# Performance work log

Measured on AMD Instinct MI355X. Metric: run time of the kernel, lower is better.

Reference implementation:

```python
import jax, jax.numpy as jnp
import numpy as np

D_MODEL = 1024
VOCAB = 32000
NUM_HEADS = 3  # MTP steps
NHEAD = 2      # attention heads per encoder layer
D_FF = 2048    # torch TransformerEncoderLayer default dim_feedforward
EPS_RMS = 1e-8
EPS_LN = 1e-5


def rmsnorm(x):
    rms = jnp.sqrt(jnp.mean(x * x, axis=-1, keepdims=True) + EPS_RMS)
    return x / rms


def layernorm(x, g, b):
    m = jnp.mean(x, axis=-1, keepdims=True)
    v = jnp.mean((x - m) ** 2, axis=-1, keepdims=True)
    return (x - m) / jnp.sqrt(v + EPS_LN) * g + b


def encoder_layer_single_token(x, p):
    # x: (..., d). Self-attention over a length-1 sequence: softmax over one key
    # gives attention weight 1, so attn_out = Wo @ (Wv @ x). Post-norm (torch default).
    v = x @ p['Wv'].T + p['bv']
    attn = v @ p['Wo'].T + p['bo']
    x = layernorm(x + attn, p['ln1_g'], p['ln1_b'])
    ff = jax.nn.relu(x @ p['W1'].T + p['b1']) @ p['W2'].T + p['b2']
    x = layernorm(x + ff, p['ln2_g'], p['ln2_b'])
    return x


def setup_inputs() -> dict:
    key = jax.random.key(0)
    ks = jax.random.split(key, 4)
    token_ids = jax.random.randint(ks[0], (4, 512), 0, VOCAB)
    embed = jax.random.normal(ks[1], (VOCAB, D_MODEL), dtype=jnp.float32) * 0.02
    s = 1.0 / np.sqrt(D_MODEL)
    params = []
    kk = ks[2]
    for k in range(NUM_HEADS):
        kk, *sub = jax.random.split(kk, 10)
        p = {
            'Wmerge': jax.random.normal(sub[0], (D_MODEL, 2 * D_MODEL)) * s,
            'bmerge': jnp.zeros((D_MODEL,)),
            'Wv': jax.random.normal(sub[1], (D_MODEL, D_MODEL)) * s,
            'bv': jnp.zeros((D_MODEL,)),
            'Wo': jax.random.normal(sub[2], (D_MODEL, D_MODEL)) * s,
            'bo': jnp.zeros((D_MODEL,)),
            'W1': jax.random.normal(sub[3], (D_FF, D_MODEL)) * s,
            'b1': jnp.zeros((D_FF,)),
            'W2': jax.random.normal(sub[4], (D_MODEL, D_FF)) * (1.0 / np.sqrt(D_FF)),
            'b2': jnp.zeros((D_MODEL,)),
            'ln1_g': jnp.ones((D_MODEL,)), 'ln1_b': jnp.zeros((D_MODEL,)),
            'ln2_g': jnp.ones((D_MODEL,)), 'ln2_b': jnp.zeros((D_MODEL,)),
        }
        params.append(p)
    # flatten params into dict entries layer{k}_{name}
    out = {'token_ids': token_ids, 'embed': embed}
    for k, p in enumerate(params):
        for name, val in p.items():
            out[f'l{k}_{name}'] = val
    return out


def _forward(token_ids, embed, layers):
    B, T = token_ids.shape
    embeds = embed[token_ids]              # (B, T, d)
    n_pos = T - NUM_HEADS                  # positions i = 0 .. T-NUM_HEADS-1
    # vectorize over i: h_prev starts as h0_seq[:, i, :] for all i at once
    idx = jnp.arange(n_pos)
    h_prev = embeds[:, idx, :]             # (B, P, d)
    logits_list = []
    for k in range(NUM_HEADS):
        p = layers[k]
        tok = embeds[:, idx + (k + 1), :]  # (B, P, d) future token embeds
        merged = jnp.concatenate([rmsnorm(h_prev), rmsnorm(tok)], axis=-1)  # (B,P,2d)
        x = merged @ p['Wmerge'].T + p['bmerge']                            # (B,P,d)
        h_curr = encoder_layer_single_token(x, p)
        logits = h_curr @ embed.T          # tied unembed (B,P,V)
        logits_list.append(logits)
        h_prev = h_curr
    # stack -> (B, P, NUM_HEADS, V) matching torch stack(dim=1) per-position then outer list
    return jnp.stack(logits_list, axis=2)


def reference(token_ids, embed,
              l0_Wmerge, l0_bmerge, l0_Wv, l0_bv, l0_Wo, l0_bo, l0_W1, l0_b1, l0_W2, l0_b2, l0_ln1_g, l0_ln1_b, l0_ln2_g, l0_ln2_b,
              l1_Wmerge, l1_bmerge, l1_Wv, l1_bv, l1_Wo, l1_bo, l1_W1, l1_b1, l1_W2, l1_b2, l1_ln1_g, l1_ln1_b, l1_ln2_g, l1_ln2_b,
              l2_Wmerge, l2_bmerge, l2_Wv, l2_bv, l2_Wo, l2_bo, l2_W1, l2_b1, l2_W2, l2_b2, l2_ln1_g, l2_ln1_b, l2_ln2_g, l2_ln2_b):
    names = ['Wmerge', 'bmerge', 'Wv', 'bv', 'Wo', 'bo', 'W1', 'b1', 'W2', 'b2', 'ln1_g', 'ln1_b', 'ln2_g', 'ln2_b']
    vals = [l0_Wmerge, l0_bmerge, l0_Wv, l0_bv, l0_Wo, l0_bo, l0_W1, l0_b1, l0_W2, l0_b2, l0_ln1_g, l0_ln1_b, l0_ln2_g, l0_ln2_b,
            l1_Wmerge, l1_bmerge, l1_Wv, l1_bv, l1_Wo, l1_bo, l1_W1, l1_b1, l1_W2, l1_b2, l1_ln1_g, l1_ln1_b, l1_ln2_g, l1_ln2_b,
            l2_Wmerge, l2_bmerge, l2_Wv, l2_bv, l2_Wo, l2_bo, l2_W1, l2_b1, l2_W2, l2_b2, l2_ln1_g, l2_ln1_b, l2_ln2_g, l2_ln2_b]
    layers = [dict(zip(names, vals[i * 14:(i + 1) * 14])) for i in range(NUM_HEADS)]
    return _forward(token_ids, embed, layers)
```

## Files before the change

### kernel.cpp

```cpp
#include <hip/hip_runtime.h>


#define NPOS   509
#define MROWS  2036
#define MPAD   2048
#define DMODEL 1024

typedef _Float16 f16;
typedef _Float16 f16x8 __attribute__((ext_vector_type(8)));
typedef _Float16 f16x4 __attribute__((ext_vector_type(4)));
typedef float    f32x4 __attribute__((ext_vector_type(4)));

#define MFMA16(a, b, c) __builtin_amdgcn_mfma_f32_16x16x32_f16(a, b, c, 0, 0, 0)
#define VM0   asm volatile("s_waitcnt vmcnt(0)" ::: "memory")
#define VM2   asm volatile("s_waitcnt vmcnt(2)" ::: "memory")
#define VM6   asm volatile("s_waitcnt vmcnt(6)" ::: "memory")
#define LGKM0 asm volatile("s_waitcnt lgkmcnt(0)" ::: "memory")
#define SCHED0 __builtin_amdgcn_sched_barrier(0)
#define BAR   asm volatile("s_barrier" ::: "memory")

__device__ __forceinline__ void gld_lds16(const void* g, void* l) {
  __builtin_amdgcn_global_load_lds(
      (const __attribute__((address_space(1))) void*)g,
      (__attribute__((address_space(3))) void*)l, 16, 0, 0);
}

__global__ __launch_bounds__(256) void conv_f32_f16(const float* __restrict__ src,
                                                    f16* __restrict__ dst, long n) {
  long i = ((long)blockIdx.x * 256 + threadIdx.x) * 8;
  if (i + 8 <= n) {
    float4 a = *(const float4*)(src + i);
    float4 b = *(const float4*)(src + i + 4);
    f16x8 o = {(f16)a.x, (f16)a.y, (f16)a.z, (f16)a.w,
               (f16)b.x, (f16)b.y, (f16)b.z, (f16)b.w};
    *(f16x8*)(dst + i) = o;
  }
}

struct ConvArgs { const float* s[12]; f16* d[12]; long n[12]; };
__global__ __launch_bounds__(256) void conv_many(ConvArgs a) {
  int t = blockIdx.y;
  long i = ((long)blockIdx.x * 256 + threadIdx.x) * 8;
  if (i + 8 <= a.n[t]) {
    const float* src = a.s[t];
    float4 x = *(const float4*)(src + i);
    float4 y = *(const float4*)(src + i + 4);
    f16x8 o = {(f16)x.x, (f16)x.y, (f16)x.z, (f16)x.w,
               (f16)y.x, (f16)y.y, (f16)y.z, (f16)y.w};
    *(f16x8*)(a.d[t] + i) = o;
  }
}

struct TpArgs { const float* s[3]; f16* d[3]; };
__global__ __launch_bounds__(256) void transpose3(TpArgs a) {
  __shared__ float t[32][33];
  int h = blockIdx.z;
  int bx = blockIdx.x * 32, by = blockIdx.y * 32;
  int tx = threadIdx.x & 31, ty = threadIdx.x >> 5;
  const float* src = a.s[h];
  f16* dst = a.d[h];
  #pragma unroll
  for (int r = 0; r < 32; r += 8)
    t[ty + r][tx] = src[(long)(by + ty + r) * 1024 + bx + tx];
  __syncthreads();
  #pragma unroll
  for (int r = 0; r < 32; r += 8)
    dst[(long)(bx + ty + r) * 1024 + by + tx] = (f16)t[tx][ty + r];
}

struct BvoArgs { const float* Wo[3]; const float* bv[3]; const float* bo[3]; float* out[3]; };
__global__ __launch_bounds__(64) void make_bvo3(BvoArgs a) {
  int h = blockIdx.y, r = blockIdx.x, l = threadIdx.x;
  const float* Wo = a.Wo[h];
  const float* bv = a.bv[h];
  float s = 0.0f;
  for (int k = l; k < 1024; k += 64) s += Wo[(long)r * 1024 + k] * bv[k];
  #pragma unroll
  for (int off = 32; off > 0; off >>= 1) s += __shfl_xor(s, off);
  if (l == 0) a.out[h][r] = s + a.bo[h][r];
}

__device__ __forceinline__ float2 block_reduce2(float a, float b) {
  #pragma unroll
  for (int off = 32; off > 0; off >>= 1) {
    a += __shfl_xor(a, off);
    b += __shfl_xor(b, off);
  }
  __shared__ float2 red[4];
  int wv = threadIdx.x >> 6;
  if ((threadIdx.x & 63) == 0) red[wv] = make_float2(a, b);
  __syncthreads();
  float2 r0 = red[0], r1 = red[1], r2 = red[2], r3 = red[3];
  return make_float2(r0.x + r1.x + r2.x + r3.x, r0.y + r1.y + r2.y + r3.y);
}

__global__ __launch_bounds__(256) void merge_rms(const float* __restrict__ hprev,
                                                 const float* __restrict__ embed,
                                                 const int* __restrict__ tok,
                                                 f16* __restrict__ merged, int koff,
                                                 int hsel) {
  int r = blockIdx.x;
  int b = r / NPOS, t = r - b * NPOS;
  int tid = threadIdx.x;
  const float* hrow = (hsel >= 0)
      ? embed + (long)tok[b * 512 + t + hsel] * DMODEL
      : hprev + (long)r * DMODEL;
  float4 hv = ((const float4*)hrow)[tid];
  float4 tv = ((const float4*)(embed + (long)tok[b * 512 + t + koff] * DMODEL))[tid];
  float sh = hv.x * hv.x + hv.y * hv.y + hv.z * hv.z + hv.w * hv.w;
  float st = tv.x * tv.x + tv.y * tv.y + tv.z * tv.z + tv.w * tv.w;
  float2 tot = block_reduce2(sh, st);
  float ih = 1.0f / sqrtf(tot.x * (1.0f / DMODEL) + 1e-8f);
  float it = 1.0f / sqrtf(tot.y * (1.0f / DMODEL) + 1e-8f);
  f16x4 oh = {(f16)(hv.x * ih), (f16)(hv.y * ih), (f16)(hv.z * ih), (f16)(hv.w * ih)};
  f16x4 ot = {(f16)(tv.x * it), (f16)(tv.y * it), (f16)(tv.z * it), (f16)(tv.w * it)};
  *(f16x4*)(merged + (long)r * 2048 + tid * 4) = oh;
  *(f16x4*)(merged + (long)r * 2048 + 1024 + tid * 4) = ot;
}

__global__ __launch_bounds__(256) void add_ln(const float* __restrict__ x,
                                              const float* __restrict__ res,
                                              const float* __restrict__ g,
                                              const float* __restrict__ bb,
                                              float* __restrict__ yf,
                                              f16* __restrict__ yh) {
  int r = blockIdx.x, tid = threadIdx.x;
  float4 a = ((const float4*)(x + (long)r * DMODEL))[tid];
  float4 c = ((const float4*)(res + (long)r * DMODEL))[tid];
  a.x += c.x; a.y += c.y; a.z += c.z; a.w += c.w;
  float s  = a.x + a.y + a.z + a.w;
  float ss = a.x * a.x + a.y * a.y + a.z * a.z + a.w * a.w;
  float2 tot = block_reduce2(s, ss);
  float mean = tot.x * (1.0f / DMODEL);
  float var  = tot.y * (1.0f / DMODEL) - mean * mean;
  float inv  = 1.0f / sqrtf(var + 1e-5f);
  float4 gv = ((const float4*)g)[tid];
  float4 bv = ((const float4*)bb)[tid];
  float y0 = (a.x - mean) * inv * gv.x + bv.x;
  float y1 = (a.y - mean) * inv * gv.y + bv.y;
  float y2 = (a.z - mean) * inv * gv.z + bv.z;
  float y3 = (a.w - mean) * inv * gv.w + bv.w;
  float4 o = {y0, y1, y2, y3};
  ((float4*)(yf + (long)r * DMODEL))[tid] = o;
  f16x4 oh = {(f16)y0, (f16)y1, (f16)y2, (f16)y3};
  *(f16x4*)(yh + (long)r * DMODEL + tid * 4) = oh;
}

template <int HAS_BIAS, int RELU, int WF32, int WF16, int MASK>
__global__ __launch_bounds__(256) void gemm_sm(const f16* __restrict__ A,
                                               const f16* __restrict__ B,
                                               const float* __restrict__ bias,
                                               float* __restrict__ Cf,
                                               f16* __restrict__ Ch,
                                               int K, int N, long ldc, long coff,
                                               int mval, long zsA, long zsB, long zsC) {
  __shared__ __align__(16) f16 sA[3][2048];
  __shared__ __align__(16) f16 sB[3][2048];
  const int tid  = threadIdx.x;
  const int lane = tid & 63, wv = tid >> 6;
  const int wm = wv >> 1, wn = wv & 1;
  const int bm = blockIdx.y, bn = blockIdx.x;
  const int lr = lane & 15, lk = lane >> 4;

  A += (long)blockIdx.z * zsA;
  B += (long)blockIdx.z * zsB;
  Ch += (long)blockIdx.z * zsC;

  const f16* gA = A + ((long)(bm * 64 + (tid >> 2))) * K + (tid & 3) * 8;
  const f16* gB = B + ((long)(bn * 64 + (tid >> 2))) * K + (tid & 3) * 8;

  const int aoff = (wm * 32 + lr) * 32 + lk * 8;
  const int boff = (wn * 32 + lr) * 32 + lk * 8;

  f32x4 acc[2][2] = {};

#define SSTAGE(buf, kt)                                \
  gld_lds16(gA + (long)(kt) * 32, &sA[buf][tid * 8]);  \
  gld_lds16(gB + (long)(kt) * 32, &sB[buf][tid * 8]);

  const int nk = K >> 5;
  SSTAGE(0, 0);
  SSTAGE(1, 1);

  int cur = 0, stg = 2;
  for (int kt = 0; kt < nk; ++kt) {
    if (kt + 1 < nk) { VM2; } else { VM0; }
    BAR;
    if (kt + 2 < nk) { SSTAGE(stg, kt + 2); }
    f16x8 af0 = *(const f16x8*)&sA[cur][aoff];
    f16x8 af1 = *(const f16x8*)&sA[cur][aoff + 512];
    f16x8 bf0 = *(const f16x8*)&sB[cur][boff];
    f16x8 bf1 = *(const f16x8*)&sB[cur][boff + 512];
    acc[0][0] = MFMA16(af0, bf0, acc[0][0]);
    acc[0][1] = MFMA16(af0, bf1, acc[0][1]);
    acc[1][0] = MFMA16(af1, bf0, acc[1][0]);
    acc[1][1] = MFMA16(af1, bf1, acc[1][1]);
    cur = cur == 2 ? 0 : cur + 1;
    stg = stg == 2 ? 0 : stg + 1;
  }
#undef SSTAGE

  const int row0 = bm * 64 + wm * 32 + lk * 4;
  const int col0 = bn * 64 + wn * 32 + lr;
  #pragma unroll
  for (int mi = 0; mi < 2; ++mi) {
    #pragma unroll
    for (int ni = 0; ni < 2; ++ni) {
      int col = col0 + ni * 16;
      float bs = HAS_BIAS ? bias[col] : 0.0f;
      #pragma unroll
      for (int rg = 0; rg < 4; ++rg) {
        int row = row0 + mi * 16 + rg;
        if (!MASK || row < mval) {
          float v = acc[mi][ni][rg] + bs;
          if (RELU) v = v > 0.0f ? v : 0.0f;
          if (WF32) Cf[(long)row * ldc + coff + col] = v;
          if (WF16) Ch[(long)row * N + col] = (f16)v;
        }
      }
    }
  }
}

__global__ __launch_bounds__(256, 2) void gemm256x(const f16* __restrict__ A,
                                                   const f16* __restrict__ B,
                                                   float* __restrict__ C) {
  __shared__ __align__(16) f16 sA[3][8192];
  __shared__ __align__(16) f16 sB[3][4096];
  const int K = 1024;
  const int tid = threadIdx.x;
  const int lane = tid & 63;
  const int wv = tid >> 6;
  const int wm = wv >> 1, wn = wv & 1;
  const int lr = lane & 15, lk = lane >> 4;

  const int flat = blockIdx.y * 250 + blockIdx.x;
  const int xcd = flat & 7, idx = flat >> 3;
  const int bm = xcd * 3 + (idx % 3);
  const int bn = idx / 3;

  const int srow = tid >> 2;
  const int schunk = (tid & 3) ^ ((tid >> 3) & 3);
  const f16* gA = A + (long)(bm * 256 + srow) * K + schunk * 8;
  const f16* gB = B + (long)(bn * 128 + srow) * K + schunk * 8;

  const int swz = ((lr >> 1) & 3) << 3;
  const int aoff = (((wm * 128 + lr) * 32) + lk * 8) ^ swz;
  const int boff = (((wn * 64  + lr) * 32) + lk * 8) ^ swz;

  f32x4 acc[8][4] = {};

#define STG_A(s, kt, i) gld_lds16(gA + (long)(kt) * 32 + (long)(i) * 64 * K, \
                                  &sA[s][(i) * 2048 + tid * 8]);
#define STG_B(s, kt, j) gld_lds16(gB + (long)(kt) * 32 + (long)(j) * 64 * K, \
                                  &sB[s][(j) * 2048 + tid * 8]);
#define STAGE_H1(s, kt) STG_A(s, kt, 0) STG_A(s, kt, 1) STG_B(s, kt, 0)
#define STAGE_H2(s, kt) STG_A(s, kt, 2) STG_A(s, kt, 3) STG_B(s, kt, 1)

  STAGE_H1(0, 0) STAGE_H2(0, 0)
  STAGE_H1(1, 1) STAGE_H2(1, 1)
  VM6; BAR;

  const int nt = 32;
  int slot = 0;
  for (int t = 0; t < nt; ++t) {
    const int s2 = (slot >= 1) ? slot - 1 : slot + 2;
    const int kt2 = (t + 2 < nt) ? (t + 2) : (t + 2 - nt);
    f16x8 alo[4], ahi[4], bf[4];

    STAGE_H1(s2, kt2)
    #pragma unroll
    for (int i = 0; i < 4; ++i) alo[i] = *(const f16x8*)&sA[slot][aoff + i * 512];
    #pragma unroll
    for (int j = 0; j < 4; ++j) bf[j] = *(const f16x8*)&sB[slot][boff + j * 512];
    LGKM0; SCHED0;
    __builtin_amdgcn_s_setprio(1);
    #pragma unroll
    for (int i = 0; i < 4; ++i)
      #pragma unroll
      for (int j = 0; j < 4; ++j)
        acc[i][j] = MFMA16(alo[i], bf[j], acc[i][j]);
    __builtin_amdgcn_s_setprio(0);
    BAR;

    STAGE_H2(s2, kt2)
    #pragma unroll
    for (int i = 0; i < 4; ++i) ahi[i] = *(const f16x8*)&sA[slot][aoff + (i + 4) * 512];
    LGKM0; SCHED0;
    __builtin_amdgcn_s_setprio(1);
    #pragma unroll
    for (int i = 0; i < 4; ++i)
      #pragma unroll
      for (int j = 0; j < 4; ++j)
        acc[i + 4][j] = MFMA16(ahi[i], bf[j], acc[i + 4][j]);
    __builtin_amdgcn_s_setprio(0);
    VM6;
    BAR;

    slot = (slot == 2) ? 0 : slot + 1;
  }
  VM0;

  const int head = bm >> 3;
  const long coff = (long)head * 32000;
  const int row0 = (bm & 7) * 256 + wm * 128 + lk * 4;
  const int col0 = bn * 128 + wn * 64 + lr;
  #pragma unroll
  for (int mi = 0; mi < 8; ++mi) {
    #pragma unroll
    for (int ni = 0; ni < 4; ++ni) {
      int col = col0 + ni * 16;
      #pragma unroll
      for (int rg = 0; rg < 4; ++rg) {
        int row = row0 + mi * 16 + rg;
        if (row < MROWS) C[(long)row * 96000 + coff + col] = acc[mi][ni][rg];
      }
    }
  }
#undef STG_A
#undef STG_B
#undef STAGE_H1
#undef STAGE_H2
}

extern "C" void kernel_launch(void* const* d_in, const int* in_sizes, int n_in,
                              void* d_out, int out_size, void* d_ws, size_t ws_size,
                              hipStream_t stream) {
  const int*   tok   = (const int*)d_in[0];
  const float* embed = (const float*)d_in[1];
  auto P = [&](int k, int j) { return (const float*)d_in[2 + k * 14 + j]; };
  float* out = (float*)d_out;

  char* w = (char*)d_ws;
  auto alloc = [&](size_t bytes) { char* p = w; w += bytes; return p; };
  const size_t MM = (size_t)1024 * 1024;

  f16* embed_h = (f16*)alloc((size_t)32000 * 1024 * 2);
  f16* Wo_all  = (f16*)alloc(3 * MM * 2);
  f16* Wvo_all = (f16*)alloc(3 * MM * 2);
  f16 *Wm_h[3], *W1_h[3], *W2_h[3];
  for (int k = 0; k < 3; ++k) {
    Wm_h[k]  = (f16*)alloc((size_t)1024 * 2048 * 2);
    W1_h[k]  = (f16*)alloc((size_t)2048 * 1024 * 2);
    W2_h[k]  = (f16*)alloc((size_t)1024 * 2048 * 2);
  }
  float* hprev  = (float*)alloc((size_t)MPAD * 1024 * 4);
  f16*   h_all  = (f16*)alloc((size_t)3 * MPAD * 1024 * 2);
  f16*   merged = (f16*)alloc((size_t)MPAD * 2048 * 2);
  float* xf     = (float*)alloc((size_t)MPAD * 1024 * 4);
  f16*   xh     = (f16*)alloc((size_t)MPAD * 1024 * 2);
  f16*   ff1    = (f16*)alloc((size_t)MPAD * 2048 * 2);
  float* t1     = (float*)alloc((size_t)MPAD * 1024 * 4);
  float* bvo    = (float*)alloc(3 * 1024 * 4);
  f16* WvT_all = merged;

  conv_f32_f16<<<16000, 256, 0, stream>>>(embed, embed_h, (long)32000 * 1024);

  ConvArgs ca;
  for (int k = 0; k < 3; ++k) {
    ca.s[k*4+0] = P(k, 0); ca.d[k*4+0] = Wm_h[k];        ca.n[k*4+0] = (long)1024 * 2048;
    ca.s[k*4+1] = P(k, 4); ca.d[k*4+1] = Wo_all + k*MM;  ca.n[k*4+1] = (long)1024 * 1024;
    ca.s[k*4+2] = P(k, 6); ca.d[k*4+2] = W1_h[k];        ca.n[k*4+2] = (long)2048 * 1024;
    ca.s[k*4+3] = P(k, 8); ca.d[k*4+3] = W2_h[k];        ca.n[k*4+3] = (long)1024 * 2048;
  }
  conv_many<<<dim3(1024, 12), 256, 0, stream>>>(ca);

  TpArgs ta;
  for (int k = 0; k < 3; ++k) { ta.s[k] = P(k, 2); ta.d[k] = WvT_all + k * MM; }
  transpose3<<<dim3(32, 32, 3), 256, 0, stream>>>(ta);

  gemm_sm<0, 0, 0, 1, 0><<<dim3(16, 16, 3), 256, 0, stream>>>(
      Wo_all, WvT_all, nullptr, nullptr, Wvo_all, 1024, 1024, 1024L, 0L, 1024,
      (long)MM, (long)MM, (long)MM);

  BvoArgs ba;
  for (int k = 0; k < 3; ++k) {
    ba.Wo[k] = P(k, 4); ba.bv[k] = P(k, 3); ba.bo[k] = P(k, 5); ba.out[k] = bvo + k * 1024;
  }
  make_bvo3<<<dim3(1024, 3), 64, 0, stream>>>(ba);

  for (int k = 0; k < 3; ++k) {
    merge_rms<<<MROWS, 256, 0, stream>>>(hprev, embed, tok, merged, k + 1,
                                         k == 0 ? 0 : -1);
    gemm_sm<1, 0, 1, 1, 0><<<dim3(16, 32), 256, 0, stream>>>(
        merged, Wm_h[k], P(k, 1), xf, xh, 2048, 1024, 1024L, 0L, MROWS, 0L, 0L, 0L);
    gemm_sm<1, 0, 1, 0, 0><<<dim3(16, 32), 256, 0, stream>>>(
        xh, Wvo_all + k * MM, bvo + k * 1024, t1, nullptr, 1024, 1024, 1024L, 0L,
        MROWS, 0L, 0L, 0L);
    add_ln<<<MROWS, 256, 0, stream>>>(xf, t1, P(k, 10), P(k, 11), xf, xh);
    gemm_sm<1, 1, 0, 1, 0><<<dim3(32, 32), 256, 0, stream>>>(
        xh, W1_h[k], P(k, 7), nullptr, ff1, 1024, 2048, 2048L, 0L, MROWS, 0L, 0L, 0L);
    gemm_sm<1, 0, 1, 0, 0><<<dim3(16, 32), 256, 0, stream>>>(
        ff1, W2_h[k], P(k, 9), t1, nullptr, 2048, 1024, 1024L, 0L, MROWS, 0L, 0L, 0L);
    add_ln<<<MROWS, 256, 0, stream>>>(xf, t1, P(k, 12), P(k, 13), hprev,
                                      h_all + (size_t)k * MPAD * 1024);
  }

  gemm256x<<<dim3(250, 24), 256, 0, stream>>>(h_all, embed_h, out);
}
```

Before: 1.112 ms.

## Enlarge vocab GEMM tile to 256x256 with 8 waves and 4-stage pipeline

The output-projection GEMM now uses 512-thread blocks computing 256x256 tiles, with a 2x4 wave layout. A 4-deep LDS ring buffer replaces the 3-deep one, leaving one barrier per k-step instead of two. The goal is to double B-tile reuse, cut global/L2 traffic per flop and lower synchronisation overhead. In exchange, LDS use grows to 128KB per block, which likely limits each CU to one block and reduces latency hiding.

```diff
diff --git a/kernel.cpp b/kernel.cpp
--- a/kernel.cpp
+++ b/kernel.cpp
@@ -14,7 +14,7 @@
 #define MFMA16(a, b, c) __builtin_amdgcn_mfma_f32_16x16x32_f16(a, b, c, 0, 0, 0)
 #define VM0   asm volatile("s_waitcnt vmcnt(0)" ::: "memory")
 #define VM2   asm volatile("s_waitcnt vmcnt(2)" ::: "memory")
-#define VM6   asm volatile("s_waitcnt vmcnt(6)" ::: "memory")
+#define VM8   asm volatile("s_waitcnt vmcnt(8)" ::: "memory")
 #define LGKM0 asm volatile("s_waitcnt lgkmcnt(0)" ::: "memory")
 #define SCHED0 __builtin_amdgcn_sched_barrier(0)
 #define BAR   asm volatile("s_barrier" ::: "memory")
@@ -222,27 +222,29 @@
   }
 }
 
-__global__ __launch_bounds__(256, 2) void gemm256x(const f16* __restrict__ A,
+__global__ __launch_bounds__(512, 2) void gemm256x(const f16* __restrict__ A,
                                                    const f16* __restrict__ B,
                                                    float* __restrict__ C) {
-  __shared__ __align__(16) f16 sA[3][8192];
-  __shared__ __align__(16) f16 sB[3][4096];
+  __shared__ __align__(16) f16 sA[4][8192];
+  __shared__ __align__(16) f16 sB[4][8192];
   const int K = 1024;
   const int tid = threadIdx.x;
   const int lane = tid & 63;
   const int wv = tid >> 6;
-  const int wm = wv >> 1, wn = wv & 1;
+  const int wm = wv >> 2, wn = wv & 3;
   const int lr = lane & 15, lk = lane >> 4;
 
-  const int flat = blockIdx.y * 250 + blockIdx.x;
-  const int xcd = flat & 7, idx = flat >> 3;
-  const int bm = xcd * 3 + (idx % 3);
-  const int bn = idx / 3;
+  const int flat = blockIdx.y * 125 + blockIdx.x;
+  const int xcd = flat & 7, i = flat >> 3;
+  const int grp = i / 15, w = i % 15;
+  const int bm = xcd * 3 + (w % 3);
+  const int bn = grp * 5 + (w / 3);
 
   const int srow = tid >> 2;
   const int schunk = (tid & 3) ^ ((tid >> 3) & 3);
   const f16* gA = A + (long)(bm * 256 + srow) * K + schunk * 8;
-  const f16* gB = B + (long)(bn * 128 + srow) * K + schunk * 8;
+  const f16* gB = B + (long)(bn * 256 + srow) * K + schunk * 8;
+  const long rstep = 128L * (long)K;
 
   const int swz = ((lr >> 1) & 3) << 3;
   const int aoff = (((wm * 128 + lr) * 32) + lk * 8) ^ swz;
@@ -250,61 +252,59 @@
 
   f32x4 acc[8][4] = {};
 
-#define STG_A(s, kt, i) gld_lds16(gA + (long)(kt) * 32 + (long)(i) * 64 * K, \
-                                  &sA[s][(i) * 2048 + tid * 8]);
-#define STG_B(s, kt, j) gld_lds16(gB + (long)(kt) * 32 + (long)(j) * 64 * K, \
-                                  &sB[s][(j) * 2048 + tid * 8]);
-#define STAGE_H1(s, kt) STG_A(s, kt, 0) STG_A(s, kt, 1) STG_B(s, kt, 0)
-#define STAGE_H2(s, kt) STG_A(s, kt, 2) STG_A(s, kt, 3) STG_B(s, kt, 1)
-
-  STAGE_H1(0, 0) STAGE_H2(0, 0)
-  STAGE_H1(1, 1) STAGE_H2(1, 1)
-  VM6; BAR;
+#define STG_A(s, kt)                                                     \
+  gld_lds16(gA + (long)(kt) * 32, &sA[s][tid * 8]);                      \
+  gld_lds16(gA + (long)(kt) * 32 + rstep, &sA[s][tid * 8 + 4096]);
+#define STG_B(s, kt)                                                     \
+  gld_lds16(gB + (long)(kt) * 32, &sB[s][tid * 8]);                      \
+  gld_lds16(gB + (long)(kt) * 32 + rstep, &sB[s][tid * 8 + 4096]);
+
+  STG_A(0, 0) STG_B(0, 0)
+  STG_A(1, 1) STG_B(1, 1)
+  STG_A(2, 2) STG_B(2, 2)
+  VM8; BAR;
 
   const int nt = 32;
-  int slot = 0;
   for (int t = 0; t < nt; ++t) {
-    const int s2 = (slot >= 1) ? slot - 1 : slot + 2;
-    const int kt2 = (t + 2 < nt) ? (t + 2) : (t + 2 - nt);
-    f16x8 alo[4], ahi[4], bf[4];
-
-    STAGE_H1(s2, kt2)
-    #pragma unroll
-    for (int i = 0; i < 4; ++i) alo[i] = *(const f16x8*)&sA[slot][aoff + i * 512];
+    const int slot = t & 3, s3 = (t + 3) & 3;
+    const int kt3 = (t + 3 < nt) ? (t + 3) : (t + 3 - nt);
+    f16x8 af[8], bf[4];
+
+    STG_A(s3, kt3)
+    #pragma unroll
+    for (int i2 = 0; i2 < 4; ++i2) af[i2] = *(const f16x8*)&sA[slot][aoff + i2 * 512];
     #pragma unroll
     for (int j = 0; j < 4; ++j) bf[j] = *(const f16x8*)&sB[slot][boff + j * 512];
     LGKM0; SCHED0;
     __builtin_amdgcn_s_setprio(1);
     #pragma unroll
-    for (int i = 0; i < 4; ++i)
+    for (int i2 = 0; i2 < 4; ++i2)
       #pragma unroll
       for (int j = 0; j < 4; ++j)
-        acc[i][j] = MFMA16(alo[i], bf[j], acc[i][j]);
+        acc[i2][j] = MFMA16(af[i2], bf[j], acc[i2][j]);
     __builtin_amdgcn_s_setprio(0);
-    BAR;
-
-    STAGE_H2(s2, kt2)
-    #pragma unroll
-    for (int i = 0; i < 4; ++i) ahi[i] = *(const f16x8*)&sA[slot][aoff + (i + 4) * 512];
+
+    STG_B(s3, kt3)
+    #pragma unroll
+    for (int i2 = 0; i2 < 4; ++i2) af[i2 + 4] = *(const f16x8*)&sA[slot][aoff + (i2 + 4) * 512];
     LGKM0; SCHED0;
     __builtin_amdgcn_s_setprio(1);
     #pragma unroll
-    for (int i = 0; i < 4; ++i)
+    for (int i2 = 0; i2 < 4; ++i2)
       #pragma unroll
       for (int j = 0; j < 4; ++j)
-        acc[i + 4][j] = MFMA16(ahi[i], bf[j], acc[i + 4][j]);
+        acc[i2 + 4][j] = MFMA16(af[i2 + 4], bf[j], acc[i2 + 4][j]);
     __builtin_amdgcn_s_setprio(0);
-    VM6;
+
+    VM8;
     BAR;
-
-    slot = (slot == 2) ? 0 : slot + 1;
   }
   VM0;
 
   const int head = bm >> 3;
   const long coff = (long)head * 32000;
   const int row0 = (bm & 7) * 256 + wm * 128 + lk * 4;
-  const int col0 = bn * 128 + wn * 64 + lr;
+  const int col0 = bn * 256 + wn * 64 + lr;
   #pragma unroll
   for (int mi = 0; mi < 8; ++mi) {
     #pragma unroll
@@ -319,8 +319,6 @@
   }
 #undef STG_A
 #undef STG_B
-#undef STAGE_H1
-#undef STAGE_H2
 }
 
 extern "C" void kernel_launch(void* const* d_in, const int* in_sizes, int n_in,
@@ -396,5 +394,5 @@
                                       h_all + (size_t)k * MPAD * 1024);
   }
 
-  gemm256x<<<dim3(250, 24), 256, 0, stream>>>(h_all, embed_h, out);
-}
+  gemm256x<<<dim3(125, 24), 512, 0, stream>>>(h_all, embed_h, out);
+}
```

Result: faster. 968.0 us (-12.9%).
